# Kernel tuning notes

Measured on AMD Instinct MI355X. Metric: run time of the kernel, lower is better.

Reference implementation:

```python
import jax, jax.numpy as jnp
import numpy as np

METAPATH = [0, 1, 2]
NUM_REL = 5
N_NODES = 50000
N_EDGES = 800000
IN_DIM = 96
HID_DIM = 96
OUT_DIM = 96
LL_DIM = 64


def setup_inputs() -> dict:
    key = jax.random.key(0)
    ks = jax.random.split(key, 12)
    x = jax.random.normal(ks[0], (N_NODES, IN_DIM), dtype=jnp.float32)
    edge_index = jax.random.randint(ks[1], (2, N_EDGES), 0, N_NODES, dtype=jnp.int64)
    edge_type = jax.random.randint(ks[2], (N_EDGES,), 0, NUM_REL, dtype=jnp.int64)
    s1 = 1.0 / np.sqrt(IN_DIM)
    s2 = 1.0 / np.sqrt(HID_DIM)
    s3 = 1.0 / np.sqrt(OUT_DIM)
    w1 = jax.random.normal(ks[3], (NUM_REL, IN_DIM, HID_DIM), dtype=jnp.float32) * s1
    root1 = jax.random.normal(ks[4], (IN_DIM, HID_DIM), dtype=jnp.float32) * s1
    b1 = jnp.zeros((HID_DIM,), dtype=jnp.float32)
    w2 = jax.random.normal(ks[5], (NUM_REL, HID_DIM, OUT_DIM), dtype=jnp.float32) * s2
    root2 = jax.random.normal(ks[6], (HID_DIM, OUT_DIM), dtype=jnp.float32) * s2
    b2 = jnp.zeros((OUT_DIM,), dtype=jnp.float32)
    lin_w = jax.random.normal(ks[7], (OUT_DIM, LL_DIM), dtype=jnp.float32) * s3
    lin_b = jnp.zeros((LL_DIM,), dtype=jnp.float32)
    return {"x": x, "edge_index": edge_index, "edge_type": edge_type,
            "w1": w1, "root1": root1, "b1": b1,
            "w2": w2, "root2": root2, "b2": b2,
            "lin_w": lin_w, "lin_b": lin_b}


def _rgcn_layer(rel, h, edge_index, edge_type, W, root, bias):
    # flow='target_to_source': message from dst node, aggregated at src node.
    src, dst = edge_index[0], edge_index[1]
    mask = (edge_type == rel)
    msg = h[dst] @ W[rel]                      # [E, out] gather + per-relation GEMM
    msg = jnp.where(mask[:, None], msg, 0.0)
    agg = jax.ops.segment_sum(msg, src, num_segments=h.shape[0])   # scatter-add
    cnt = jax.ops.segment_sum(mask.astype(h.dtype), src, num_segments=h.shape[0])
    agg = agg / jnp.clip(cnt, 1.0)[:, None]    # mean normalization per target
    return agg + h @ root + bias


def reference(x, edge_index, edge_type, w1, root1, b1, w2, root2, b2, lin_w, lin_b):
    h = x
    for layer_index, rel in enumerate(METAPATH):
        if layer_index == 0:
            h = jax.nn.relu(_rgcn_layer(rel, h, edge_index, edge_type, w1, root1, b1))
        else:
            h = jax.nn.relu(_rgcn_layer(rel, h, edge_index, edge_type, w2, root2, b2))
    return h @ lin_w + lin_b
```

## Files before the change

### kernel.cpp

```cpp
#include <hip/hip_runtime.h>

#define NNODES 50000
#define NEDGES 800000
#define DIM 96
#define LLDIM 64
#define NRELS 3
#define SCAN_N (NRELS * NNODES)

#define BT_PLANE 18432
#define BT_LAYER (2 * BT_PLANE)
#define BTL_PLANE 6144
#define BT_LIN_OFF (3 * BT_LAYER)

typedef __attribute__((ext_vector_type(8))) short bf16x8;
typedef __attribute__((ext_vector_type(4))) float f32x4;

__device__ __forceinline__ unsigned short f2bf(float x) {
    union { float f; unsigned u; } v; v.f = x;
    unsigned r = v.u + 0x7fffu + ((v.u >> 16) & 1u);
    return (unsigned short)(r >> 16);
}
__device__ __forceinline__ float bf2f(unsigned short b) {
    union { unsigned u; float f; } v; v.u = ((unsigned)b) << 16;
    return v.f;
}


__global__ void hist_kernel(const int* __restrict__ ei, const int* __restrict__ et,
                            int* __restrict__ deg) {
    int e = blockIdx.x * 256 + threadIdx.x;
    if (e >= NEDGES) return;
    int r = et[e];
    if (r < NRELS) atomicAdd(&deg[r * NNODES + ei[e]], 1);
}

__global__ void scan1_kernel(const int* __restrict__ in, int* __restrict__ out,
                             int* __restrict__ partials, int n) {
    __shared__ int sdata[256];
    int tid = threadIdx.x;
    int base = blockIdx.x * 1024 + tid * 4;
    int v0 = (base + 0 < n) ? in[base + 0] : 0;
    int v1 = (base + 1 < n) ? in[base + 1] : 0;
    int v2 = (base + 2 < n) ? in[base + 2] : 0;
    int v3 = (base + 3 < n) ? in[base + 3] : 0;
    int tsum = v0 + v1 + v2 + v3;
    sdata[tid] = tsum;
    __syncthreads();
    for (int off = 1; off < 256; off <<= 1) {
        int x = sdata[tid];
        int y = (tid >= off) ? sdata[tid - off] : 0;
        __syncthreads();
        sdata[tid] = x + y;
        __syncthreads();
    }
    int excl = sdata[tid] - tsum;
    if (tid == 255) partials[blockIdx.x] = sdata[255];
    if (base + 0 < n) out[base + 0] = excl;
    excl += v0;
    if (base + 1 < n) out[base + 1] = excl;
    excl += v1;
    if (base + 2 < n) out[base + 2] = excl;
    excl += v2;
    if (base + 3 < n) out[base + 3] = excl;
}

__global__ void scan2_kernel(int* __restrict__ partials, int nb) {
    __shared__ int sdata[256];
    int tid = threadIdx.x;
    int v = (tid < nb) ? partials[tid] : 0;
    sdata[tid] = v;
    __syncthreads();
    for (int off = 1; off < 256; off <<= 1) {
        int x = sdata[tid];
        int y = (tid >= off) ? sdata[tid - off] : 0;
        __syncthreads();
        sdata[tid] = x + y;
        __syncthreads();
    }
    partials[tid] = sdata[tid] - v;
}

__global__ void scan3_kernel(int* __restrict__ out, int* __restrict__ cursor,
                             const int* __restrict__ partials, int n) {
    int idx = blockIdx.x * 256 + threadIdx.x;
    if (idx < n) {
        int v = out[idx] + partials[idx >> 10];
        out[idx] = v;
        cursor[idx] = v;
    }
}

__global__ void fill_kernel(const int* __restrict__ ei, const int* __restrict__ et,
                            int* __restrict__ cursor, int* __restrict__ col) {
    int e = blockIdx.x * 256 + threadIdx.x;
    if (e >= NEDGES) return;
    int r = et[e];
    if (r < NRELS) {
        int pos = atomicAdd(&cursor[r * NNODES + ei[e]], 1);
        col[pos] = ei[NEDGES + e];
    }
}


__global__ void prep_kernel(const float* __restrict__ w1, const float* __restrict__ root1,
                            const float* __restrict__ w2, const float* __restrict__ root2,
                            const float* __restrict__ lin_w,
                            unsigned short* __restrict__ bt, int* __restrict__ deg) {
    int idx = blockIdx.x * 256 + threadIdx.x;
    if (idx < SCAN_N) deg[idx] = 0;
    const int LYR = 96 * 192;
    if (idx < 3 * LYR) {
        int l = idx / LYR;
        int rem = idx % LYR;
        int c = rem / 192;
        int k = rem % 192;
        const float* Wm;
        const float* Rm;
        if (l == 0) { Wm = w1; Rm = root1; }
        else        { Wm = w2 + (size_t)l * 96 * 96; Rm = root2; }
        float v = (k < 96) ? Wm[(size_t)k * 96 + c] : Rm[(size_t)(k - 96) * 96 + c];
        unsigned short hi = f2bf(v);
        unsigned short lo = f2bf(v - bf2f(hi));
        int ph = k / 96, kk = k % 96;
        int ks = kk / 32, g = (kk & 31) >> 3, kr = k & 7;
        int cg = c >> 4, r = c & 15;
        size_t off = (((size_t)((ph * 3 + ks) * 6 + cg)) * 64 + g * 16 + r) * 8 + kr;
        unsigned short* base = bt + (size_t)l * BT_LAYER;
        base[off] = hi;
        base[BT_PLANE + off] = lo;
    } else if (idx < 3 * LYR + 64 * 96) {
        int rem = idx - 3 * LYR;
        int c = rem / 96;
        int k = rem % 96;
        float v = lin_w[(size_t)k * 64 + c];
        unsigned short hi = f2bf(v);
        unsigned short lo = f2bf(v - bf2f(hi));
        int ks = k / 32, g = (k & 31) >> 3, kr = k & 7;
        int cg = c >> 4, r = c & 15;
        size_t off = (((size_t)(ks * 4 + cg)) * 64 + g * 16 + r) * 8 + kr;
        unsigned short* base = bt + BT_LIN_OFF;
        base[off] = hi;
        base[BTL_PLANE + off] = lo;
    }
}


__device__ __forceinline__ void gather_to_lds(
    const float* __restrict__ h, const int* __restrict__ rs, const int* __restrict__ re,
    const int* __restrict__ col, int n0, int tid,
    unsigned short* Ah, unsigned short* Al) {
    const int nd = tid >> 2;
    const int node = n0 + nd;
    const int cq4 = (tid & 3) * 24;
    float a[24];
#pragma unroll
    for (int j = 0; j < 24; ++j) a[j] = 0.0f;
    int s = 0, e = 0;
    if (node < NNODES) { s = rs[node]; e = re[node]; }
    for (int i = s; i < e; ++i) {
        int d = col[i];
        const float* p = h + (size_t)d * DIM + cq4;
#pragma unroll
        for (int j6 = 0; j6 < 6; ++j6) {
            float4 v = *(const float4*)(p + j6 * 4);
            a[j6 * 4 + 0] += v.x; a[j6 * 4 + 1] += v.y;
            a[j6 * 4 + 2] += v.z; a[j6 * 4 + 3] += v.w;
        }
    }
    float scl = 1.0f / fmaxf((float)(e - s), 1.0f);
    int arow = nd * 104 + cq4;
#pragma unroll
    for (int jp = 0; jp < 12; ++jp) {
        float v0 = a[jp * 2] * scl, v1 = a[jp * 2 + 1] * scl;
        unsigned short h0 = f2bf(v0), h1 = f2bf(v1);
        unsigned short l0 = f2bf(v0 - bf2f(h0)), l1 = f2bf(v1 - bf2f(h1));
        *(unsigned int*)&Ah[arow + jp * 2] = (unsigned)h0 | ((unsigned)h1 << 16);
        *(unsigned int*)&Al[arow + jp * 2] = (unsigned)l0 | ((unsigned)l1 << 16);
    }
}

__device__ __forceinline__ void stage_h_to_lds(
    const float* __restrict__ src, int n0, int tid,
    unsigned short* Ah, unsigned short* Al) {
#pragma unroll
    for (int j = 0; j < 6; ++j) {
        int idx = tid + j * 256;
        int nd = idx / 24;
        int kq = idx % 24;
        int node = n0 + nd;
        if (node >= NNODES) node = NNODES - 1;
        float4 v = *(const float4*)(src + (size_t)node * DIM + kq * 4);
        unsigned short h0 = f2bf(v.x), h1 = f2bf(v.y), h2 = f2bf(v.z), h3 = f2bf(v.w);
        *(ushort4*)&Ah[nd * 104 + kq * 4] = make_ushort4(h0, h1, h2, h3);
        unsigned short l0 = f2bf(v.x - bf2f(h0));
        unsigned short l1 = f2bf(v.y - bf2f(h1));
        unsigned short l2 = f2bf(v.z - bf2f(h2));
        unsigned short l3 = f2bf(v.w - bf2f(h3));
        *(ushort4*)&Al[nd * 104 + kq * 4] = make_ushort4(l0, l1, l2, l3);
    }
}

#define KS_LOOP(PH)                                                                     \
    _Pragma("unroll")                                                                   \
    for (int ks = 0; ks < 3; ++ks) {                                                    \
        const int ko = ks * 32 + g * 8;                                                 \
        bf16x8 a0h = *(const bf16x8*)&Ah[(rb_base + r) * 104 + ko];                     \
        bf16x8 a1h = *(const bf16x8*)&Ah[(rb_base + 16 + r) * 104 + ko];                \
        bf16x8 a0l = *(const bf16x8*)&Al[(rb_base + r) * 104 + ko];                     \
        bf16x8 a1l = *(const bf16x8*)&Al[(rb_base + 16 + r) * 104 + ko];                \
        const unsigned short* bks = bt + ((size_t)(((PH) * 3 + ks) * 6) * 64 + lane) * 8;\
        _Pragma("unroll")                                                               \
        for (int ct = 0; ct < 3; ++ct) {                                                \
            const unsigned short* bp = bks + (size_t)(cg_base + ct) * 512;              \
            bf16x8 bhv = *(const bf16x8*)bp;                                            \
            bf16x8 blv = *(const bf16x8*)(bp + BT_PLANE);                               \
            acc[0][ct] = __builtin_amdgcn_mfma_f32_16x16x32_bf16(a0h, bhv, acc[0][ct], 0, 0, 0); \
            acc[1][ct] = __builtin_amdgcn_mfma_f32_16x16x32_bf16(a1h, bhv, acc[1][ct], 0, 0, 0); \
            acc[0][ct] = __builtin_amdgcn_mfma_f32_16x16x32_bf16(a0l, bhv, acc[0][ct], 0, 0, 0); \
            acc[1][ct] = __builtin_amdgcn_mfma_f32_16x16x32_bf16(a1l, bhv, acc[1][ct], 0, 0, 0); \
            acc[0][ct] = __builtin_amdgcn_mfma_f32_16x16x32_bf16(a0h, blv, acc[0][ct], 0, 0, 0); \
            acc[1][ct] = __builtin_amdgcn_mfma_f32_16x16x32_bf16(a1h, blv, acc[1][ct], 0, 0, 0); \
        }                                                                               \
    }

__global__ __launch_bounds__(256) void layer_fused_kernel(
    const float* __restrict__ h, const int* __restrict__ rs, const int* __restrict__ re,
    const int* __restrict__ col, const unsigned short* __restrict__ bt,
    const float* __restrict__ b, float* __restrict__ out) {
    __shared__ unsigned short Ah[64 * 104];
    __shared__ unsigned short Al[64 * 104];
    const int tid = threadIdx.x;
    const int lane = tid & 63;
    const int w = tid >> 6;
    const int r = lane & 15;
    const int g = lane >> 4;
    const int rb_base = (w >> 1) * 32;
    const int cg_base = (w & 1) * 3;
    const int n0 = blockIdx.x * 64;

    gather_to_lds(h, rs, re, col, n0, tid, Ah, Al);

    f32x4 acc[2][3];
#pragma unroll
    for (int i = 0; i < 2; ++i)
#pragma unroll
        for (int j = 0; j < 3; ++j) acc[i][j] = (f32x4){0.f, 0.f, 0.f, 0.f};

    __syncthreads();
    KS_LOOP(0)
    __syncthreads();
    stage_h_to_lds(h, n0, tid, Ah, Al);
    __syncthreads();
    KS_LOOP(1)

#pragma unroll
    for (int ct = 0; ct < 3; ++ct) {
        int colc = (cg_base + ct) * 16 + r;
        float bias = b[colc];
#pragma unroll
        for (int rbi = 0; rbi < 2; ++rbi) {
            int row0 = n0 + rb_base + rbi * 16 + g * 4;
#pragma unroll
            for (int j = 0; j < 4; ++j) {
                int node = row0 + j;
                if (node < NNODES)
                    out[(size_t)node * DIM + colc] = fmaxf(acc[rbi][ct][j] + bias, 0.0f);
            }
        }
    }
}


__global__ __launch_bounds__(256) void layer2_final_kernel(
    const float* __restrict__ h, const int* __restrict__ rs, const int* __restrict__ re,
    const int* __restrict__ col, const unsigned short* __restrict__ bt,
    const float* __restrict__ b, const unsigned short* __restrict__ btl,
    const float* __restrict__ LB, float* __restrict__ out) {
    __shared__ unsigned short Ah[64 * 104];
    __shared__ unsigned short Al[64 * 104];
    const int tid = threadIdx.x;
    const int lane = tid & 63;
    const int w = tid >> 6;
    const int r = lane & 15;
    const int g = lane >> 4;
    const int rb_base = (w >> 1) * 32;
    const int cg_base = (w & 1) * 3;
    const int n0 = blockIdx.x * 64;

    gather_to_lds(h, rs, re, col, n0, tid, Ah, Al);

    f32x4 acc[2][3];
#pragma unroll
    for (int i = 0; i < 2; ++i)
#pragma unroll
        for (int j = 0; j < 3; ++j) acc[i][j] = (f32x4){0.f, 0.f, 0.f, 0.f};

    __syncthreads();
    KS_LOOP(0)
    __syncthreads();
    stage_h_to_lds(h, n0, tid, Ah, Al);
    __syncthreads();
    KS_LOOP(1)

    __syncthreads();
#pragma unroll
    for (int ct = 0; ct < 3; ++ct) {
        int colc = (cg_base + ct) * 16 + r;
        float bias = b[colc];
#pragma unroll
        for (int rbi = 0; rbi < 2; ++rbi) {
            int row0 = rb_base + rbi * 16 + g * 4;
#pragma unroll
            for (int j = 0; j < 4; ++j) {
                float v = fmaxf(acc[rbi][ct][j] + bias, 0.0f);
                unsigned short hh = f2bf(v);
                unsigned short ll = f2bf(v - bf2f(hh));
                Ah[(row0 + j) * 104 + colc] = hh;
                Al[(row0 + j) * 104 + colc] = ll;
            }
        }
    }
    __syncthreads();

    const int cgf = (w & 1) * 2;
    f32x4 accf[2][2];
#pragma unroll
    for (int i = 0; i < 2; ++i)
#pragma unroll
        for (int j = 0; j < 2; ++j) accf[i][j] = (f32x4){0.f, 0.f, 0.f, 0.f};

#pragma unroll
    for (int ks = 0; ks < 3; ++ks) {
        const int ko = ks * 32 + g * 8;
        bf16x8 a0h = *(const bf16x8*)&Ah[(rb_base + r) * 104 + ko];
        bf16x8 a1h = *(const bf16x8*)&Ah[(rb_base + 16 + r) * 104 + ko];
        bf16x8 a0l = *(const bf16x8*)&Al[(rb_base + r) * 104 + ko];
        bf16x8 a1l = *(const bf16x8*)&Al[(rb_base + 16 + r) * 104 + ko];
        const unsigned short* bks = btl + ((size_t)(ks * 4) * 64 + lane) * 8;
#pragma unroll
        for (int ct = 0; ct < 2; ++ct) {
            const unsigned short* bp = bks + (size_t)(cgf + ct) * 512;
            bf16x8 bhv = *(const bf16x8*)bp;
            bf16x8 blv = *(const bf16x8*)(bp + BTL_PLANE);
            accf[0][ct] = __builtin_amdgcn_mfma_f32_16x16x32_bf16(a0h, bhv, accf[0][ct], 0, 0, 0);
            accf[1][ct] = __builtin_amdgcn_mfma_f32_16x16x32_bf16(a1h, bhv, accf[1][ct], 0, 0, 0);
            accf[0][ct] = __builtin_amdgcn_mfma_f32_16x16x32_bf16(a0l, bhv, accf[0][ct], 0, 0, 0);
            accf[1][ct] = __builtin_amdgcn_mfma_f32_16x16x32_bf16(a1l, bhv, accf[1][ct], 0, 0, 0);
            accf[0][ct] = __builtin_amdgcn_mfma_f32_16x16x32_bf16(a0h, blv, accf[0][ct], 0, 0, 0);
            accf[1][ct] = __builtin_amdgcn_mfma_f32_16x16x32_bf16(a1h, blv, accf[1][ct], 0, 0, 0);
        }
    }

#pragma unroll
    for (int ct = 0; ct < 2; ++ct) {
        int colc = (cgf + ct) * 16 + r;
        float bias = LB[colc];
#pragma unroll
        for (int rbi = 0; rbi < 2; ++rbi) {
            int row0 = n0 + rb_base + rbi * 16 + g * 4;
#pragma unroll
            for (int j = 0; j < 4; ++j) {
                int node = row0 + j;
                if (node < NNODES)
                    out[(size_t)node * LLDIM + colc] = accf[rbi][ct][j] + bias;
            }
        }
    }
}

extern "C" void kernel_launch(void* const* d_in, const int* in_sizes, int n_in,
                              void* d_out, int out_size, void* d_ws, size_t ws_size,
                              hipStream_t stream) {
    const float* x     = (const float*)d_in[0];
    const int*   ei    = (const int*)d_in[1];
    const int*   et    = (const int*)d_in[2];
    const float* w1    = (const float*)d_in[3];
    const float* root1 = (const float*)d_in[4];
    const float* b1    = (const float*)d_in[5];
    const float* w2    = (const float*)d_in[6];
    const float* root2 = (const float*)d_in[7];
    const float* b2    = (const float*)d_in[8];
    const float* lin_w = (const float*)d_in[9];
    const float* lin_b = (const float*)d_in[10];

    float* bufA = (float*)d_ws;
    float* bufB = bufA + (size_t)NNODES * DIM;
    int* deg       = (int*)(bufB + (size_t)NNODES * DIM);
    int* row_start = deg + SCAN_N;
    int* row_end   = row_start + SCAN_N;
    int* col       = row_end + SCAN_N;
    int* partials  = col + NEDGES;
    unsigned short* bt = (unsigned short*)(partials + 256);

    const int edge_blocks = (NEDGES + 255) / 256;
    const int scan_blocks = (SCAN_N + 1023) / 1024;
    const int node_tiles  = (NNODES + 63) / 64;
    const int prep_blocks = (SCAN_N + 255) / 256;

    prep_kernel<<<prep_blocks, 256, 0, stream>>>(w1, root1, w2, root2, lin_w, bt, deg);

    hist_kernel<<<edge_blocks, 256, 0, stream>>>(ei, et, deg);
    scan1_kernel<<<scan_blocks, 256, 0, stream>>>(deg, row_start, partials, SCAN_N);
    scan2_kernel<<<1, 256, 0, stream>>>(partials, scan_blocks);
    scan3_kernel<<<(SCAN_N + 255) / 256, 256, 0, stream>>>(row_start, row_end, partials, SCAN_N);
    fill_kernel<<<edge_blocks, 256, 0, stream>>>(ei, et, row_end, col);

    layer_fused_kernel<<<node_tiles, 256, 0, stream>>>(
        x, row_start + 0 * NNODES, row_end + 0 * NNODES, col,
        bt + 0 * (size_t)BT_LAYER, b1, bufA);

    layer_fused_kernel<<<node_tiles, 256, 0, stream>>>(
        bufA, row_start + 1 * NNODES, row_end + 1 * NNODES, col,
        bt + 1 * (size_t)BT_LAYER, b2, bufB);

    layer2_final_kernel<<<node_tiles, 256, 0, stream>>>(
        bufB, row_start + 2 * NNODES, row_end + 2 * NNODES, col,
        bt + 2 * (size_t)BT_LAYER, b2, bt + BT_LIN_OFF, lin_b, (float*)d_out);
}
```

Measured before the change: 221.3 us.

## Double threads per node tile and unroll neighbor gather by two

The three layer kernels now launch 512 threads per 64-node tile instead of 256. Each node's gather is split across 8 threads with 12 columns each, and the edge loop is unrolled by two with separate accumulators so more loads are in flight. The MFMA work per wave drops to one 16-row block. This aims to raise memory-level parallelism in the latency-bound neighbor gather, at the cost of more waves competing for the same LDS tile and redundant B-fragment loads per wave.

```diff
diff --git a/kernel.cpp b/kernel.cpp
--- a/kernel.cpp
+++ b/kernel.cpp
@@ -149,28 +149,46 @@
     const float* __restrict__ h, const int* __restrict__ rs, const int* __restrict__ re,
     const int* __restrict__ col, int n0, int tid,
     unsigned short* Ah, unsigned short* Al) {
-    const int nd = tid >> 2;
+    const int nd = tid >> 3;
     const int node = n0 + nd;
-    const int cq4 = (tid & 3) * 24;
-    float a[24];
-#pragma unroll
-    for (int j = 0; j < 24; ++j) a[j] = 0.0f;
+    const int cq = (tid & 7) * 12;
+    float a[12], b[12];
+#pragma unroll
+    for (int j = 0; j < 12; ++j) { a[j] = 0.0f; b[j] = 0.0f; }
     int s = 0, e = 0;
     if (node < NNODES) { s = rs[node]; e = re[node]; }
-    for (int i = s; i < e; ++i) {
+    int i = s;
+    for (; i + 2 <= e; i += 2) {
+        int d0 = col[i];
+        int d1 = col[i + 1];
+        const float* p0 = h + (size_t)d0 * DIM + cq;
+        const float* p1 = h + (size_t)d1 * DIM + cq;
+#pragma unroll
+        for (int j4 = 0; j4 < 3; ++j4) {
+            float4 v0 = *(const float4*)(p0 + j4 * 4);
+            float4 v1 = *(const float4*)(p1 + j4 * 4);
+            a[j4 * 4 + 0] += v0.x; a[j4 * 4 + 1] += v0.y;
+            a[j4 * 4 + 2] += v0.z; a[j4 * 4 + 3] += v0.w;
+            b[j4 * 4 + 0] += v1.x; b[j4 * 4 + 1] += v1.y;
+            b[j4 * 4 + 2] += v1.z; b[j4 * 4 + 3] += v1.w;
+        }
+    }
+    if (i < e) {
         int d = col[i];
-        const float* p = h + (size_t)d * DIM + cq4;
-#pragma unroll
-        for (int j6 = 0; j6 < 6; ++j6) {
-            float4 v = *(const float4*)(p + j6 * 4);
-            a[j6 * 4 + 0] += v.x; a[j6 * 4 + 1] += v.y;
-            a[j6 * 4 + 2] += v.z; a[j6 * 4 + 3] += v.w;
-        }
-    }
+        const float* p = h + (size_t)d * DIM + cq;
+#pragma unroll
+        for (int j4 = 0; j4 < 3; ++j4) {
+            float4 v = *(const float4*)(p + j4 * 4);
+            a[j4 * 4 + 0] += v.x; a[j4 * 4 + 1] += v.y;
+            a[j4 * 4 + 2] += v.z; a[j4 * 4 + 3] += v.w;
+        }
+    }
+#pragma unroll
+    for (int j = 0; j < 12; ++j) a[j] += b[j];
     float scl = 1.0f / fmaxf((float)(e - s), 1.0f);
-    int arow = nd * 104 + cq4;
-#pragma unroll
-    for (int jp = 0; jp < 12; ++jp) {
+    int arow = nd * 104 + cq;
+#pragma unroll
+    for (int jp = 0; jp < 6; ++jp) {
         float v0 = a[jp * 2] * scl, v1 = a[jp * 2 + 1] * scl;
         unsigned short h0 = f2bf(v0), h1 = f2bf(v1);
         unsigned short l0 = f2bf(v0 - bf2f(h0)), l1 = f2bf(v1 - bf2f(h1));
@@ -183,8 +201,8 @@
     const float* __restrict__ src, int n0, int tid,
     unsigned short* Ah, unsigned short* Al) {
 #pragma unroll
-    for (int j = 0; j < 6; ++j) {
-        int idx = tid + j * 256;
+    for (int j = 0; j < 3; ++j) {
+        int idx = tid + j * 512;
         int nd = idx / 24;
         int kq = idx % 24;
         int node = n0 + nd;
@@ -205,25 +223,20 @@
     for (int ks = 0; ks < 3; ++ks) {                                                    \
         const int ko = ks * 32 + g * 8;                                                 \
         bf16x8 a0h = *(const bf16x8*)&Ah[(rb_base + r) * 104 + ko];                     \
-        bf16x8 a1h = *(const bf16x8*)&Ah[(rb_base + 16 + r) * 104 + ko];                \
         bf16x8 a0l = *(const bf16x8*)&Al[(rb_base + r) * 104 + ko];                     \
-        bf16x8 a1l = *(const bf16x8*)&Al[(rb_base + 16 + r) * 104 + ko];                \
         const unsigned short* bks = bt + ((size_t)(((PH) * 3 + ks) * 6) * 64 + lane) * 8;\
         _Pragma("unroll")                                                               \
         for (int ct = 0; ct < 3; ++ct) {                                                \
             const unsigned short* bp = bks + (size_t)(cg_base + ct) * 512;              \
             bf16x8 bhv = *(const bf16x8*)bp;                                            \
             bf16x8 blv = *(const bf16x8*)(bp + BT_PLANE);                               \
-            acc[0][ct] = __builtin_amdgcn_mfma_f32_16x16x32_bf16(a0h, bhv, acc[0][ct], 0, 0, 0); \
-            acc[1][ct] = __builtin_amdgcn_mfma_f32_16x16x32_bf16(a1h, bhv, acc[1][ct], 0, 0, 0); \
-            acc[0][ct] = __builtin_amdgcn_mfma_f32_16x16x32_bf16(a0l, bhv, acc[0][ct], 0, 0, 0); \
-            acc[1][ct] = __builtin_amdgcn_mfma_f32_16x16x32_bf16(a1l, bhv, acc[1][ct], 0, 0, 0); \
-            acc[0][ct] = __builtin_amdgcn_mfma_f32_16x16x32_bf16(a0h, blv, acc[0][ct], 0, 0, 0); \
-            acc[1][ct] = __builtin_amdgcn_mfma_f32_16x16x32_bf16(a1h, blv, acc[1][ct], 0, 0, 0); \
+            acc[ct] = __builtin_amdgcn_mfma_f32_16x16x32_bf16(a0h, bhv, acc[ct], 0, 0, 0); \
+            acc[ct] = __builtin_amdgcn_mfma_f32_16x16x32_bf16(a0l, bhv, acc[ct], 0, 0, 0); \
+            acc[ct] = __builtin_amdgcn_mfma_f32_16x16x32_bf16(a0h, blv, acc[ct], 0, 0, 0); \
         }                                                                               \
     }
 
-__global__ __launch_bounds__(256) void layer_fused_kernel(
+__global__ __launch_bounds__(512, 4) void layer_fused_kernel(
     const float* __restrict__ h, const int* __restrict__ rs, const int* __restrict__ re,
     const int* __restrict__ col, const unsigned short* __restrict__ bt,
     const float* __restrict__ b, float* __restrict__ out) {
@@ -234,17 +247,15 @@
     const int w = tid >> 6;
     const int r = lane & 15;
     const int g = lane >> 4;
-    const int rb_base = (w >> 1) * 32;
+    const int rb_base = (w >> 1) * 16;
     const int cg_base = (w & 1) * 3;
     const int n0 = blockIdx.x * 64;
 
     gather_to_lds(h, rs, re, col, n0, tid, Ah, Al);
 
-    f32x4 acc[2][3];
-#pragma unroll
-    for (int i = 0; i < 2; ++i)
-#pragma unroll
-        for (int j = 0; j < 3; ++j) acc[i][j] = (f32x4){0.f, 0.f, 0.f, 0.f};
+    f32x4 acc[3];
+#pragma unroll
+    for (int j = 0; j < 3; ++j) acc[j] = (f32x4){0.f, 0.f, 0.f, 0.f};
 
     __syncthreads();
     KS_LOOP(0)
@@ -257,21 +268,18 @@
     for (int ct = 0; ct < 3; ++ct) {
         int colc = (cg_base + ct) * 16 + r;
         float bias = b[colc];
-#pragma unroll
-        for (int rbi = 0; rbi < 2; ++rbi) {
-            int row0 = n0 + rb_base + rbi * 16 + g * 4;
-#pragma unroll
-            for (int j = 0; j < 4; ++j) {
-                int node = row0 + j;
-                if (node < NNODES)
-                    out[(size_t)node * DIM + colc] = fmaxf(acc[rbi][ct][j] + bias, 0.0f);
-            }
-        }
-    }
-}
-
-
-__global__ __launch_bounds__(256) void layer2_final_kernel(
+        int row0 = n0 + rb_base + g * 4;
+#pragma unroll
+        for (int j = 0; j < 4; ++j) {
+            int node = row0 + j;
+            if (node < NNODES)
+                out[(size_t)node * DIM + colc] = fmaxf(acc[ct][j] + bias, 0.0f);
+        }
+    }
+}
+
+
+__global__ __launch_bounds__(512, 4) void layer2_final_kernel(
     const float* __restrict__ h, const int* __restrict__ rs, const int* __restrict__ re,
     const int* __restrict__ col, const unsigned short* __restrict__ bt,
     const float* __restrict__ b, const unsigned short* __restrict__ btl,
@@ -283,17 +291,15 @@
     const int w = tid >> 6;
     const int r = lane & 15;
     const int g = lane >> 4;
-    const int rb_base = (w >> 1) * 32;
+    const int rb_base = (w >> 1) * 16;
     const int cg_base = (w & 1) * 3;
     const int n0 = blockIdx.x * 64;
 
     gather_to_lds(h, rs, re, col, n0, tid, Ah, Al);
 
-    f32x4 acc[2][3];
-#pragma unroll
-    for (int i = 0; i < 2; ++i)
-#pragma unroll
-        for (int j = 0; j < 3; ++j) acc[i][j] = (f32x4){0.f, 0.f, 0.f, 0.f};
+    f32x4 acc[3];
+#pragma unroll
+    for (int j = 0; j < 3; ++j) acc[j] = (f32x4){0.f, 0.f, 0.f, 0.f};
 
     __syncthreads();
     KS_LOOP(0)
@@ -307,47 +313,37 @@
     for (int ct = 0; ct < 3; ++ct) {
         int colc = (cg_base + ct) * 16 + r;
         float bias = b[colc];
-#pragma unroll
-        for (int rbi = 0; rbi < 2; ++rbi) {
-            int row0 = rb_base + rbi * 16 + g * 4;
-#pragma unroll
-            for (int j = 0; j < 4; ++j) {
-                float v = fmaxf(acc[rbi][ct][j] + bias, 0.0f);
-                unsigned short hh = f2bf(v);
-                unsigned short ll = f2bf(v - bf2f(hh));
-                Ah[(row0 + j) * 104 + colc] = hh;
-                Al[(row0 + j) * 104 + colc] = ll;
-            }
+        int row0 = rb_base + g * 4;
+#pragma unroll
+        for (int j = 0; j < 4; ++j) {
+            float v = fmaxf(acc[ct][j] + bias, 0.0f);
+            unsigned short hh = f2bf(v);
+            unsigned short ll = f2bf(v - bf2f(hh));
+            Ah[(row0 + j) * 104 + colc] = hh;
+            Al[(row0 + j) * 104 + colc] = ll;
         }
     }
     __syncthreads();
 
     const int cgf = (w & 1) * 2;
-    f32x4 accf[2][2];
-#pragma unroll
-    for (int i = 0; i < 2; ++i)
-#pragma unroll
-        for (int j = 0; j < 2; ++j) accf[i][j] = (f32x4){0.f, 0.f, 0.f, 0.f};
+    f32x4 accf[2];
+#pragma unroll
+    for (int j = 0; j < 2; ++j) accf[j] = (f32x4){0.f, 0.f, 0.f, 0.f};
 
 #pragma unroll
     for (int ks = 0; ks < 3; ++ks) {
         const int ko = ks * 32 + g * 8;
         bf16x8 a0h = *(const bf16x8*)&Ah[(rb_base + r) * 104 + ko];
-        bf16x8 a1h = *(const bf16x8*)&Ah[(rb_base + 16 + r) * 104 + ko];
         bf16x8 a0l = *(const bf16x8*)&Al[(rb_base + r) * 104 + ko];
-        bf16x8 a1l = *(const bf16x8*)&Al[(rb_base + 16 + r) * 104 + ko];
         const unsigned short* bks = btl + ((size_t)(ks * 4) * 64 + lane) * 8;
 #pragma unroll
         for (int ct = 0; ct < 2; ++ct) {
             const unsigned short* bp = bks + (size_t)(cgf + ct) * 512;
             bf16x8 bhv = *(const bf16x8*)bp;
             bf16x8 blv = *(const bf16x8*)(bp + BTL_PLANE);
-            accf[0][ct] = __builtin_amdgcn_mfma_f32_16x16x32_bf16(a0h, bhv, accf[0][ct], 0, 0, 0);
-            accf[1][ct] = __builtin_amdgcn_mfma_f32_16x16x32_bf16(a1h, bhv, accf[1][ct], 0, 0, 0);
-            accf[0][ct] = __builtin_amdgcn_mfma_f32_16x16x32_bf16(a0l, bhv, accf[0][ct], 0, 0, 0);
-            accf[1][ct] = __builtin_amdgcn_mfma_f32_16x16x32_bf16(a1l, bhv, accf[1][ct], 0, 0, 0);
-            accf[0][ct] = __builtin_amdgcn_mfma_f32_16x16x32_bf16(a0h, blv, accf[0][ct], 0, 0, 0);
-            accf[1][ct] = __builtin_amdgcn_mfma_f32_16x16x32_bf16(a1h, blv, accf[1][ct], 0, 0, 0);
+            accf[ct] = __builtin_amdgcn_mfma_f32_16x16x32_bf16(a0h, bhv, accf[ct], 0, 0, 0);
+            accf[ct] = __builtin_amdgcn_mfma_f32_16x16x32_bf16(a0l, bhv, accf[ct], 0, 0, 0);
+            accf[ct] = __builtin_amdgcn_mfma_f32_16x16x32_bf16(a0h, blv, accf[ct], 0, 0, 0);
         }
     }
 
@@ -355,15 +351,12 @@
     for (int ct = 0; ct < 2; ++ct) {
         int colc = (cgf + ct) * 16 + r;
         float bias = LB[colc];
-#pragma unroll
-        for (int rbi = 0; rbi < 2; ++rbi) {
-            int row0 = n0 + rb_base + rbi * 16 + g * 4;
-#pragma unroll
-            for (int j = 0; j < 4; ++j) {
-                int node = row0 + j;
-                if (node < NNODES)
-                    out[(size_t)node * LLDIM + colc] = accf[rbi][ct][j] + bias;
-            }
+        int row0 = n0 + rb_base + g * 4;
+#pragma unroll
+        for (int j = 0; j < 4; ++j) {
+            int node = row0 + j;
+            if (node < NNODES)
+                out[(size_t)node * LLDIM + colc] = accf[ct][j] + bias;
         }
     }
 }
@@ -405,15 +398,15 @@
     scan3_kernel<<<(SCAN_N + 255) / 256, 256, 0, stream>>>(row_start, row_end, partials, SCAN_N);
     fill_kernel<<<edge_blocks, 256, 0, stream>>>(ei, et, row_end, col);
 
-    layer_fused_kernel<<<node_tiles, 256, 0, stream>>>(
+    layer_fused_kernel<<<node_tiles, 512, 0, stream>>>(
         x, row_start + 0 * NNODES, row_end + 0 * NNODES, col,
         bt + 0 * (size_t)BT_LAYER, b1, bufA);
 
-    layer_fused_kernel<<<node_tiles, 256, 0, stream>>>(
+    layer_fused_kernel<<<node_tiles, 512, 0, stream>>>(
         bufA, row_start + 1 * NNODES, row_end + 1 * NNODES, col,
         bt + 1 * (size_t)BT_LAYER, b2, bufB);
 
-    layer2_final_kernel<<<node_tiles, 256, 0, stream>>>(
+    layer2_final_kernel<<<node_tiles, 512, 0, stream>>>(
         bufB, row_start + 2 * NNODES, row_end + 2 * NNODES, col,
         bt + 2 * (size_t)BT_LAYER, b2, bt + BT_LIN_OFF, lin_b, (float*)d_out);
 }
```

New measurement: 232.2 us. 1.05x slower.

## Load root operand directly from global into MFMA registers and drop scan2 kernel

Applied to the files above, without the earlier changes.

The self (root) GEMM phase no longer stages h into LDS with two extra barriers. Each lane loads its A fragments straight from global memory and splits them into bf16 hi/lo in registers. Separately, the single-block scan2 launch is removed: each scan3 block now reduces the preceding block partials itself, which saves a kernel launch at the cost of redundant reductions. The direct loads are less coalesced (8 floats per lane per row) and repeat across the two column-group waves.

```diff
diff --git a/kernel.cpp b/kernel.cpp
--- a/kernel.cpp
+++ b/kernel.cpp
@@ -23,6 +23,16 @@
 __device__ __forceinline__ float bf2f(unsigned short b) {
     union { unsigned u; float f; } v; v.u = ((unsigned)b) << 16;
     return v.f;
+}
+__device__ __forceinline__ void f8_to_bf(const float* f, bf16x8& hv, bf16x8& lv) {
+    union { bf16x8 v; unsigned short u[8]; } H, L;
+#pragma unroll
+    for (int j = 0; j < 8; ++j) {
+        unsigned short hh = f2bf(f[j]);
+        H.u[j] = hh;
+        L.u[j] = f2bf(f[j] - bf2f(hh));
+    }
+    hv = H.v; lv = L.v;
 }
 
 
@@ -64,27 +74,21 @@
     if (base + 3 < n) out[base + 3] = excl;
 }
 
-__global__ void scan2_kernel(int* __restrict__ partials, int nb) {
+__global__ void scan3_kernel(int* __restrict__ out, int* __restrict__ cursor,
+                             const int* __restrict__ partials, int n) {
     __shared__ int sdata[256];
     int tid = threadIdx.x;
-    int v = (tid < nb) ? partials[tid] : 0;
-    sdata[tid] = v;
-    __syncthreads();
-    for (int off = 1; off < 256; off <<= 1) {
-        int x = sdata[tid];
-        int y = (tid >= off) ? sdata[tid - off] : 0;
+    int c = blockIdx.x >> 2;
+    sdata[tid] = (tid < c) ? partials[tid] : 0;
+    __syncthreads();
+    for (int off = 128; off > 0; off >>= 1) {
+        if (tid < off) sdata[tid] += sdata[tid + off];
         __syncthreads();
-        sdata[tid] = x + y;
-        __syncthreads();
-    }
-    partials[tid] = sdata[tid] - v;
-}
-
-__global__ void scan3_kernel(int* __restrict__ out, int* __restrict__ cursor,
-                             const int* __restrict__ partials, int n) {
-    int idx = blockIdx.x * 256 + threadIdx.x;
+    }
+    int base = sdata[0];
+    int idx = blockIdx.x * 256 + tid;
     if (idx < n) {
-        int v = out[idx] + partials[idx >> 10];
+        int v = out[idx] + base;
         out[idx] = v;
         cursor[idx] = v;
     }
@@ -179,28 +183,7 @@
     }
 }
 
-__device__ __forceinline__ void stage_h_to_lds(
-    const float* __restrict__ src, int n0, int tid,
-    unsigned short* Ah, unsigned short* Al) {
-#pragma unroll
-    for (int j = 0; j < 6; ++j) {
-        int idx = tid + j * 256;
-        int nd = idx / 24;
-        int kq = idx % 24;
-        int node = n0 + nd;
-        if (node >= NNODES) node = NNODES - 1;
-        float4 v = *(const float4*)(src + (size_t)node * DIM + kq * 4);
-        unsigned short h0 = f2bf(v.x), h1 = f2bf(v.y), h2 = f2bf(v.z), h3 = f2bf(v.w);
-        *(ushort4*)&Ah[nd * 104 + kq * 4] = make_ushort4(h0, h1, h2, h3);
-        unsigned short l0 = f2bf(v.x - bf2f(h0));
-        unsigned short l1 = f2bf(v.y - bf2f(h1));
-        unsigned short l2 = f2bf(v.z - bf2f(h2));
-        unsigned short l3 = f2bf(v.w - bf2f(h3));
-        *(ushort4*)&Al[nd * 104 + kq * 4] = make_ushort4(l0, l1, l2, l3);
-    }
-}
-
-#define KS_LOOP(PH)                                                                     \
+#define KS_LOOP0                                                                        \
     _Pragma("unroll")                                                                   \
     for (int ks = 0; ks < 3; ++ks) {                                                    \
         const int ko = ks * 32 + g * 8;                                                 \
@@ -208,7 +191,34 @@
         bf16x8 a1h = *(const bf16x8*)&Ah[(rb_base + 16 + r) * 104 + ko];                \
         bf16x8 a0l = *(const bf16x8*)&Al[(rb_base + r) * 104 + ko];                     \
         bf16x8 a1l = *(const bf16x8*)&Al[(rb_base + 16 + r) * 104 + ko];                \
-        const unsigned short* bks = bt + ((size_t)(((PH) * 3 + ks) * 6) * 64 + lane) * 8;\
+        const unsigned short* bks = bt + ((size_t)(ks * 6) * 64 + lane) * 8;            \
+        _Pragma("unroll")                                                               \
+        for (int ct = 0; ct < 3; ++ct) {                                                \
+            const unsigned short* bp = bks + (size_t)(cg_base + ct) * 512;              \
+            bf16x8 bhv = *(const bf16x8*)bp;                                            \
+            bf16x8 blv = *(const bf16x8*)(bp + BT_PLANE);                               \
+            acc[0][ct] = __builtin_amdgcn_mfma_f32_16x16x32_bf16(a0h, bhv, acc[0][ct], 0, 0, 0); \
+            acc[1][ct] = __builtin_amdgcn_mfma_f32_16x16x32_bf16(a1h, bhv, acc[1][ct], 0, 0, 0); \
+            acc[0][ct] = __builtin_amdgcn_mfma_f32_16x16x32_bf16(a0l, bhv, acc[0][ct], 0, 0, 0); \
+            acc[1][ct] = __builtin_amdgcn_mfma_f32_16x16x32_bf16(a1l, bhv, acc[1][ct], 0, 0, 0); \
+            acc[0][ct] = __builtin_amdgcn_mfma_f32_16x16x32_bf16(a0h, blv, acc[0][ct], 0, 0, 0); \
+            acc[1][ct] = __builtin_amdgcn_mfma_f32_16x16x32_bf16(a1h, blv, acc[1][ct], 0, 0, 0); \
+        }                                                                               \
+    }
+
+#define KS_LOOP1                                                                        \
+    _Pragma("unroll")                                                                   \
+    for (int ks = 0; ks < 3; ++ks) {                                                    \
+        const int ko = ks * 32 + g * 8;                                                 \
+        float f0[8], f1[8];                                                             \
+        *(float4*)&f0[0] = *(const float4*)(h + (size_t)row0g * DIM + ko);              \
+        *(float4*)&f0[4] = *(const float4*)(h + (size_t)row0g * DIM + ko + 4);          \
+        *(float4*)&f1[0] = *(const float4*)(h + (size_t)row1g * DIM + ko);              \
+        *(float4*)&f1[4] = *(const float4*)(h + (size_t)row1g * DIM + ko + 4);          \
+        bf16x8 a0h, a0l, a1h, a1l;                                                      \
+        f8_to_bf(f0, a0h, a0l);                                                         \
+        f8_to_bf(f1, a1h, a1l);                                                         \
+        const unsigned short* bks = bt + ((size_t)((3 + ks) * 6) * 64 + lane) * 8;      \
         _Pragma("unroll")                                                               \
         for (int ct = 0; ct < 3; ++ct) {                                                \
             const unsigned short* bp = bks + (size_t)(cg_base + ct) * 512;              \
@@ -246,12 +256,12 @@
 #pragma unroll
         for (int j = 0; j < 3; ++j) acc[i][j] = (f32x4){0.f, 0.f, 0.f, 0.f};
 
-    __syncthreads();
-    KS_LOOP(0)
-    __syncthreads();
-    stage_h_to_lds(h, n0, tid, Ah, Al);
-    __syncthreads();
-    KS_LOOP(1)
+    int row0g = n0 + rb_base + r;      if (row0g >= NNODES) row0g = NNODES - 1;
+    int row1g = n0 + rb_base + 16 + r; if (row1g >= NNODES) row1g = NNODES - 1;
+
+    __syncthreads();
+    KS_LOOP0
+    KS_LOOP1
 
 #pragma unroll
     for (int ct = 0; ct < 3; ++ct) {
@@ -295,12 +305,12 @@
 #pragma unroll
         for (int j = 0; j < 3; ++j) acc[i][j] = (f32x4){0.f, 0.f, 0.f, 0.f};
 
-    __syncthreads();
-    KS_LOOP(0)
-    __syncthreads();
-    stage_h_to_lds(h, n0, tid, Ah, Al);
-    __syncthreads();
-    KS_LOOP(1)
+    int row0g = n0 + rb_base + r;      if (row0g >= NNODES) row0g = NNODES - 1;
+    int row1g = n0 + rb_base + 16 + r; if (row1g >= NNODES) row1g = NNODES - 1;
+
+    __syncthreads();
+    KS_LOOP0
+    KS_LOOP1
 
     __syncthreads();
 #pragma unroll
@@ -401,7 +411,6 @@
 
     hist_kernel<<<edge_blocks, 256, 0, stream>>>(ei, et, deg);
     scan1_kernel<<<scan_blocks, 256, 0, stream>>>(deg, row_start, partials, SCAN_N);
-    scan2_kernel<<<1, 256, 0, stream>>>(partials, scan_blocks);
     scan3_kernel<<<(SCAN_N + 255) / 256, 256, 0, stream>>>(row_start, row_end, partials, SCAN_N);
     fill_kernel<<<edge_blocks, 256, 0, stream>>>(ei, et, row_end, col);
 
```

New measurement: 229.8 us. +3.8%, slower.

## Double layer block threads, split gather across edges, run root and message GEMMs in parallel

Applied to the files above, without the earlier changes.

The fused layer kernels now launch 512 threads per 64-node tile. Each node's edge list is split between two thread groups and the partial sums are combined with a shuffle. Half the waves compute the aggregated-message GEMM while the other half compute the root GEMM at the same time, and the two results are reduced through LDS, which removes the serialized second phase. The scan2 kernel is folded into scan3, where each block reduces the preceding block partials itself, and the final linear layer is spread across 8 waves. This costs twice the LDS per block and an extra reduction sync, which may lower occupancy.

```diff
diff --git a/kernel.cpp b/kernel.cpp
--- a/kernel.cpp
+++ b/kernel.cpp
@@ -64,27 +64,21 @@
     if (base + 3 < n) out[base + 3] = excl;
 }
 
-__global__ void scan2_kernel(int* __restrict__ partials, int nb) {
+__global__ void scan3_kernel(int* __restrict__ out, int* __restrict__ cursor,
+                             const int* __restrict__ partials, int n) {
     __shared__ int sdata[256];
     int tid = threadIdx.x;
-    int v = (tid < nb) ? partials[tid] : 0;
-    sdata[tid] = v;
-    __syncthreads();
-    for (int off = 1; off < 256; off <<= 1) {
-        int x = sdata[tid];
-        int y = (tid >= off) ? sdata[tid - off] : 0;
+    int c = blockIdx.x >> 2;
+    sdata[tid] = (tid < c) ? partials[tid] : 0;
+    __syncthreads();
+    for (int off = 128; off > 0; off >>= 1) {
+        if (tid < off) sdata[tid] += sdata[tid + off];
         __syncthreads();
-        sdata[tid] = x + y;
-        __syncthreads();
-    }
-    partials[tid] = sdata[tid] - v;
-}
-
-__global__ void scan3_kernel(int* __restrict__ out, int* __restrict__ cursor,
-                             const int* __restrict__ partials, int n) {
-    int idx = blockIdx.x * 256 + threadIdx.x;
+    }
+    int base = sdata[0];
+    int idx = blockIdx.x * 256 + tid;
     if (idx < n) {
-        int v = out[idx] + partials[idx >> 10];
+        int v = out[idx] + base;
         out[idx] = v;
         cursor[idx] = v;
     }
@@ -145,21 +139,44 @@
 }
 
 
-__device__ __forceinline__ void gather_to_lds(
+__device__ __forceinline__ void stage_h_512(
+    const float* __restrict__ h, int n0, int tid,
+    unsigned short* Hh, unsigned short* Hl) {
+#pragma unroll
+    for (int j = 0; j < 3; ++j) {
+        int idx = tid + j * 512;
+        int nd = idx / 24;
+        int kq = idx % 24;
+        int node = n0 + nd;
+        if (node >= NNODES) node = NNODES - 1;
+        float4 v = *(const float4*)(h + (size_t)node * DIM + kq * 4);
+        unsigned short h0 = f2bf(v.x), h1 = f2bf(v.y), h2 = f2bf(v.z), h3 = f2bf(v.w);
+        *(ushort4*)&Hh[nd * 104 + kq * 4] = make_ushort4(h0, h1, h2, h3);
+        unsigned short l0 = f2bf(v.x - bf2f(h0));
+        unsigned short l1 = f2bf(v.y - bf2f(h1));
+        unsigned short l2 = f2bf(v.z - bf2f(h2));
+        unsigned short l3 = f2bf(v.w - bf2f(h3));
+        *(ushort4*)&Hl[nd * 104 + kq * 4] = make_ushort4(l0, l1, l2, l3);
+    }
+}
+
+__device__ __forceinline__ void gather_512(
     const float* __restrict__ h, const int* __restrict__ rs, const int* __restrict__ re,
     const int* __restrict__ col, int n0, int tid,
-    unsigned short* Ah, unsigned short* Al) {
-    const int nd = tid >> 2;
+    unsigned short* Gh, unsigned short* Gl) {
+    const int nd = tid >> 3;
     const int node = n0 + nd;
-    const int cq4 = (tid & 3) * 24;
+    const int j = tid & 7;
+    const int cq = (j & 3) * 24;
+    const int es = j >> 2;
     float a[24];
 #pragma unroll
-    for (int j = 0; j < 24; ++j) a[j] = 0.0f;
+    for (int m = 0; m < 24; ++m) a[m] = 0.0f;
     int s = 0, e = 0;
     if (node < NNODES) { s = rs[node]; e = re[node]; }
-    for (int i = s; i < e; ++i) {
+    for (int i = s + es; i < e; i += 2) {
         int d = col[i];
-        const float* p = h + (size_t)d * DIM + cq4;
+        const float* p = h + (size_t)d * DIM + cq;
 #pragma unroll
         for (int j6 = 0; j6 < 6; ++j6) {
             float4 v = *(const float4*)(p + j6 * 4);
@@ -167,47 +184,29 @@
             a[j6 * 4 + 2] += v.z; a[j6 * 4 + 3] += v.w;
         }
     }
+#pragma unroll
+    for (int m = 0; m < 24; ++m) a[m] += __shfl_xor(a[m], 4);
     float scl = 1.0f / fmaxf((float)(e - s), 1.0f);
-    int arow = nd * 104 + cq4;
-#pragma unroll
-    for (int jp = 0; jp < 12; ++jp) {
-        float v0 = a[jp * 2] * scl, v1 = a[jp * 2 + 1] * scl;
+    const int cb = es * 12;
+    int arow = nd * 104 + cq + cb;
+#pragma unroll
+    for (int jp = 0; jp < 6; ++jp) {
+        float v0 = a[cb + jp * 2] * scl, v1 = a[cb + jp * 2 + 1] * scl;
         unsigned short h0 = f2bf(v0), h1 = f2bf(v1);
         unsigned short l0 = f2bf(v0 - bf2f(h0)), l1 = f2bf(v1 - bf2f(h1));
-        *(unsigned int*)&Ah[arow + jp * 2] = (unsigned)h0 | ((unsigned)h1 << 16);
-        *(unsigned int*)&Al[arow + jp * 2] = (unsigned)l0 | ((unsigned)l1 << 16);
-    }
-}
-
-__device__ __forceinline__ void stage_h_to_lds(
-    const float* __restrict__ src, int n0, int tid,
-    unsigned short* Ah, unsigned short* Al) {
-#pragma unroll
-    for (int j = 0; j < 6; ++j) {
-        int idx = tid + j * 256;
-        int nd = idx / 24;
-        int kq = idx % 24;
-        int node = n0 + nd;
-        if (node >= NNODES) node = NNODES - 1;
-        float4 v = *(const float4*)(src + (size_t)node * DIM + kq * 4);
-        unsigned short h0 = f2bf(v.x), h1 = f2bf(v.y), h2 = f2bf(v.z), h3 = f2bf(v.w);
-        *(ushort4*)&Ah[nd * 104 + kq * 4] = make_ushort4(h0, h1, h2, h3);
-        unsigned short l0 = f2bf(v.x - bf2f(h0));
-        unsigned short l1 = f2bf(v.y - bf2f(h1));
-        unsigned short l2 = f2bf(v.z - bf2f(h2));
-        unsigned short l3 = f2bf(v.w - bf2f(h3));
-        *(ushort4*)&Al[nd * 104 + kq * 4] = make_ushort4(l0, l1, l2, l3);
-    }
-}
-
-#define KS_LOOP(PH)                                                                     \
+        *(unsigned int*)&Gh[arow + jp * 2] = (unsigned)h0 | ((unsigned)h1 << 16);
+        *(unsigned int*)&Gl[arow + jp * 2] = (unsigned)l0 | ((unsigned)l1 << 16);
+    }
+}
+
+#define KS_PHASE(AH, AL, PH)                                                            \
     _Pragma("unroll")                                                                   \
     for (int ks = 0; ks < 3; ++ks) {                                                    \
         const int ko = ks * 32 + g * 8;                                                 \
-        bf16x8 a0h = *(const bf16x8*)&Ah[(rb_base + r) * 104 + ko];                     \
-        bf16x8 a1h = *(const bf16x8*)&Ah[(rb_base + 16 + r) * 104 + ko];                \
-        bf16x8 a0l = *(const bf16x8*)&Al[(rb_base + r) * 104 + ko];                     \
-        bf16x8 a1l = *(const bf16x8*)&Al[(rb_base + 16 + r) * 104 + ko];                \
+        bf16x8 a0h = *(const bf16x8*)&AH[(rb_base + r) * 104 + ko];                     \
+        bf16x8 a1h = *(const bf16x8*)&AH[(rb_base + 16 + r) * 104 + ko];                \
+        bf16x8 a0l = *(const bf16x8*)&AL[(rb_base + r) * 104 + ko];                     \
+        bf16x8 a1l = *(const bf16x8*)&AL[(rb_base + 16 + r) * 104 + ko];                \
         const unsigned short* bks = bt + ((size_t)(((PH) * 3 + ks) * 6) * 64 + lane) * 8;\
         _Pragma("unroll")                                                               \
         for (int ct = 0; ct < 3; ++ct) {                                                \
@@ -223,22 +222,28 @@
         }                                                                               \
     }
 
-__global__ __launch_bounds__(256) void layer_fused_kernel(
+__global__ __launch_bounds__(512) void layer_fused_kernel(
     const float* __restrict__ h, const int* __restrict__ rs, const int* __restrict__ re,
     const int* __restrict__ col, const unsigned short* __restrict__ bt,
     const float* __restrict__ b, float* __restrict__ out) {
-    __shared__ unsigned short Ah[64 * 104];
-    __shared__ unsigned short Al[64 * 104];
+    __shared__ unsigned short SM[4 * 64 * 104];
+    unsigned short* Gh = SM;
+    unsigned short* Gl = SM + 6656;
+    unsigned short* Hh = SM + 2 * 6656;
+    unsigned short* Hl = SM + 3 * 6656;
     const int tid = threadIdx.x;
     const int lane = tid & 63;
     const int w = tid >> 6;
+    const int wq = w & 3;
+    const int pp = w >> 2;
     const int r = lane & 15;
     const int g = lane >> 4;
-    const int rb_base = (w >> 1) * 32;
-    const int cg_base = (w & 1) * 3;
+    const int rb_base = (wq >> 1) * 32;
+    const int cg_base = (wq & 1) * 3;
     const int n0 = blockIdx.x * 64;
 
-    gather_to_lds(h, rs, re, col, n0, tid, Ah, Al);
+    stage_h_512(h, n0, tid, Hh, Hl);
+    gather_512(h, rs, re, col, n0, tid, Gh, Gl);
 
     f32x4 acc[2][3];
 #pragma unroll
@@ -247,47 +252,76 @@
         for (int j = 0; j < 3; ++j) acc[i][j] = (f32x4){0.f, 0.f, 0.f, 0.f};
 
     __syncthreads();
-    KS_LOOP(0)
-    __syncthreads();
-    stage_h_to_lds(h, n0, tid, Ah, Al);
-    __syncthreads();
-    KS_LOOP(1)
-
-#pragma unroll
-    for (int ct = 0; ct < 3; ++ct) {
-        int colc = (cg_base + ct) * 16 + r;
-        float bias = b[colc];
-#pragma unroll
-        for (int rbi = 0; rbi < 2; ++rbi) {
-            int row0 = n0 + rb_base + rbi * 16 + g * 4;
-#pragma unroll
-            for (int j = 0; j < 4; ++j) {
-                int node = row0 + j;
-                if (node < NNODES)
-                    out[(size_t)node * DIM + colc] = fmaxf(acc[rbi][ct][j] + bias, 0.0f);
+    if (pp == 0) { KS_PHASE(Gh, Gl, 0) }
+    else         { KS_PHASE(Hh, Hl, 1) }
+    __syncthreads();
+
+    float* X = (float*)SM;
+    if (pp) {
+        int t = tid - 256;
+#pragma unroll
+        for (int i = 0; i < 2; ++i)
+#pragma unroll
+            for (int ct = 0; ct < 3; ++ct) {
+                int o = t * 26 + (i * 3 + ct) * 4;
+                *(float2*)&X[o]     = make_float2(acc[i][ct][0], acc[i][ct][1]);
+                *(float2*)&X[o + 2] = make_float2(acc[i][ct][2], acc[i][ct][3]);
+            }
+    }
+    __syncthreads();
+    if (pp == 0) {
+#pragma unroll
+        for (int i = 0; i < 2; ++i)
+#pragma unroll
+            for (int ct = 0; ct < 3; ++ct) {
+                int o = tid * 26 + (i * 3 + ct) * 4;
+                float2 u0 = *(float2*)&X[o];
+                float2 u1 = *(float2*)&X[o + 2];
+                acc[i][ct][0] += u0.x; acc[i][ct][1] += u0.y;
+                acc[i][ct][2] += u1.x; acc[i][ct][3] += u1.y;
+            }
+#pragma unroll
+        for (int ct = 0; ct < 3; ++ct) {
+            int colc = (cg_base + ct) * 16 + r;
+            float bias = b[colc];
+#pragma unroll
+            for (int rbi = 0; rbi < 2; ++rbi) {
+                int row0 = n0 + rb_base + rbi * 16 + g * 4;
+#pragma unroll
+                for (int j = 0; j < 4; ++j) {
+                    int node = row0 + j;
+                    if (node < NNODES)
+                        out[(size_t)node * DIM + colc] = fmaxf(acc[rbi][ct][j] + bias, 0.0f);
+                }
             }
         }
     }
 }
 
 
-__global__ __launch_bounds__(256) void layer2_final_kernel(
+__global__ __launch_bounds__(512) void layer2_final_kernel(
     const float* __restrict__ h, const int* __restrict__ rs, const int* __restrict__ re,
     const int* __restrict__ col, const unsigned short* __restrict__ bt,
     const float* __restrict__ b, const unsigned short* __restrict__ btl,
     const float* __restrict__ LB, float* __restrict__ out) {
-    __shared__ unsigned short Ah[64 * 104];
-    __shared__ unsigned short Al[64 * 104];
+    __shared__ unsigned short SM[4 * 64 * 104];
+    unsigned short* Gh = SM;
+    unsigned short* Gl = SM + 6656;
+    unsigned short* Hh = SM + 2 * 6656;
+    unsigned short* Hl = SM + 3 * 6656;
     const int tid = threadIdx.x;
     const int lane = tid & 63;
     const int w = tid >> 6;
+    const int wq = w & 3;
+    const int pp = w >> 2;
     const int r = lane & 15;
     const int g = lane >> 4;
-    const int rb_base = (w >> 1) * 32;
-    const int cg_base = (w & 1) * 3;
+    const int rb_base = (wq >> 1) * 32;
+    const int cg_base = (wq & 1) * 3;
     const int n0 = blockIdx.x * 64;
 
-    gather_to_lds(h, rs, re, col, n0, tid, Ah, Al);
+    stage_h_512(h, n0, tid, Hh, Hl);
+    gather_512(h, rs, re, col, n0, tid, Gh, Gl);
 
     f32x4 acc[2][3];
 #pragma unroll
@@ -296,73 +330,84 @@
         for (int j = 0; j < 3; ++j) acc[i][j] = (f32x4){0.f, 0.f, 0.f, 0.f};
 
     __syncthreads();
-    KS_LOOP(0)
-    __syncthreads();
-    stage_h_to_lds(h, n0, tid, Ah, Al);
-    __syncthreads();
-    KS_LOOP(1)
-
-    __syncthreads();
-#pragma unroll
-    for (int ct = 0; ct < 3; ++ct) {
-        int colc = (cg_base + ct) * 16 + r;
-        float bias = b[colc];
-#pragma unroll
-        for (int rbi = 0; rbi < 2; ++rbi) {
-            int row0 = rb_base + rbi * 16 + g * 4;
-#pragma unroll
-            for (int j = 0; j < 4; ++j) {
-                float v = fmaxf(acc[rbi][ct][j] + bias, 0.0f);
-                unsigned short hh = f2bf(v);
-                unsigned short ll = f2bf(v - bf2f(hh));
-                Ah[(row0 + j) * 104 + colc] = hh;
-                Al[(row0 + j) * 104 + colc] = ll;
+    if (pp == 0) { KS_PHASE(Gh, Gl, 0) }
+    else         { KS_PHASE(Hh, Hl, 1) }
+    __syncthreads();
+
+    float* X = (float*)SM;
+    if (pp) {
+        int t = tid - 256;
+#pragma unroll
+        for (int i = 0; i < 2; ++i)
+#pragma unroll
+            for (int ct = 0; ct < 3; ++ct) {
+                int o = t * 26 + (i * 3 + ct) * 4;
+                *(float2*)&X[o]     = make_float2(acc[i][ct][0], acc[i][ct][1]);
+                *(float2*)&X[o + 2] = make_float2(acc[i][ct][2], acc[i][ct][3]);
+            }
+    }
+    __syncthreads();
+    if (pp == 0) {
+#pragma unroll
+        for (int ct = 0; ct < 3; ++ct) {
+            int colc = (cg_base + ct) * 16 + r;
+            float bias = b[colc];
+#pragma unroll
+            for (int rbi = 0; rbi < 2; ++rbi) {
+                int o = tid * 26 + (rbi * 3 + ct) * 4;
+                float2 u0 = *(float2*)&X[o];
+                float2 u1 = *(float2*)&X[o + 2];
+                float vv[4] = {acc[rbi][ct][0] + u0.x, acc[rbi][ct][1] + u0.y,
+                               acc[rbi][ct][2] + u1.x, acc[rbi][ct][3] + u1.y};
+                int row0 = rb_base + rbi * 16 + g * 4;
+#pragma unroll
+                for (int j = 0; j < 4; ++j) {
+                    float v = fmaxf(vv[j] + bias, 0.0f);
+                    unsigned short hh = f2bf(v);
+                    unsigned short ll = f2bf(v - bf2f(hh));
+                    Hh[(row0 + j) * 104 + colc] = hh;
+                    Hl[(row0 + j) * 104 + colc] = ll;
+                }
             }
         }
     }
     __syncthreads();
 
-    const int cgf = (w & 1) * 2;
-    f32x4 accf[2][2];
-#pragma unroll
-    for (int i = 0; i < 2; ++i)
-#pragma unroll
-        for (int j = 0; j < 2; ++j) accf[i][j] = (f32x4){0.f, 0.f, 0.f, 0.f};
+    const int rbf = (w >> 2) * 32;
+    const int cgf = w & 3;
+    f32x4 accf[2];
+#pragma unroll
+    for (int j = 0; j < 2; ++j) accf[j] = (f32x4){0.f, 0.f, 0.f, 0.f};
 
 #pragma unroll
     for (int ks = 0; ks < 3; ++ks) {
         const int ko = ks * 32 + g * 8;
-        bf16x8 a0h = *(const bf16x8*)&Ah[(rb_base + r) * 104 + ko];
-        bf16x8 a1h = *(const bf16x8*)&Ah[(rb_base + 16 + r) * 104 + ko];
-        bf16x8 a0l = *(const bf16x8*)&Al[(rb_base + r) * 104 + ko];
-        bf16x8 a1l = *(const bf16x8*)&Al[(rb_base + 16 + r) * 104 + ko];
-        const unsigned short* bks = btl + ((size_t)(ks * 4) * 64 + lane) * 8;
-#pragma unroll
-        for (int ct = 0; ct < 2; ++ct) {
-            const unsigned short* bp = bks + (size_t)(cgf + ct) * 512;
-            bf16x8 bhv = *(const bf16x8*)bp;
-            bf16x8 blv = *(const bf16x8*)(bp + BTL_PLANE);
-            accf[0][ct] = __builtin_amdgcn_mfma_f32_16x16x32_bf16(a0h, bhv, accf[0][ct], 0, 0, 0);
-            accf[1][ct] = __builtin_amdgcn_mfma_f32_16x16x32_bf16(a1h, bhv, accf[1][ct], 0, 0, 0);
-            accf[0][ct] = __builtin_amdgcn_mfma_f32_16x16x32_bf16(a0l, bhv, accf[0][ct], 0, 0, 0);
-            accf[1][ct] = __builtin_amdgcn_mfma_f32_16x16x32_bf16(a1l, bhv, accf[1][ct], 0, 0, 0);
-            accf[0][ct] = __builtin_amdgcn_mfma_f32_16x16x32_bf16(a0h, blv, accf[0][ct], 0, 0, 0);
-            accf[1][ct] = __builtin_amdgcn_mfma_f32_16x16x32_bf16(a1h, blv, accf[1][ct], 0, 0, 0);
-        }
-    }
-
-#pragma unroll
-    for (int ct = 0; ct < 2; ++ct) {
-        int colc = (cgf + ct) * 16 + r;
+        bf16x8 a0h = *(const bf16x8*)&Hh[(rbf + r) * 104 + ko];
+        bf16x8 a1h = *(const bf16x8*)&Hh[(rbf + 16 + r) * 104 + ko];
+        bf16x8 a0l = *(const bf16x8*)&Hl[(rbf + r) * 104 + ko];
+        bf16x8 a1l = *(const bf16x8*)&Hl[(rbf + 16 + r) * 104 + ko];
+        const unsigned short* bp = btl + ((size_t)(ks * 4 + cgf) * 64 + lane) * 8;
+        bf16x8 bhv = *(const bf16x8*)bp;
+        bf16x8 blv = *(const bf16x8*)(bp + BTL_PLANE);
+        accf[0] = __builtin_amdgcn_mfma_f32_16x16x32_bf16(a0h, bhv, accf[0], 0, 0, 0);
+        accf[1] = __builtin_amdgcn_mfma_f32_16x16x32_bf16(a1h, bhv, accf[1], 0, 0, 0);
+        accf[0] = __builtin_amdgcn_mfma_f32_16x16x32_bf16(a0l, bhv, accf[0], 0, 0, 0);
+        accf[1] = __builtin_amdgcn_mfma_f32_16x16x32_bf16(a1l, bhv, accf[1], 0, 0, 0);
+        accf[0] = __builtin_amdgcn_mfma_f32_16x16x32_bf16(a0h, blv, accf[0], 0, 0, 0);
+        accf[1] = __builtin_amdgcn_mfma_f32_16x16x32_bf16(a1h, blv, accf[1], 0, 0, 0);
+    }
+
+    {
+        int colc = cgf * 16 + r;
         float bias = LB[colc];
 #pragma unroll
         for (int rbi = 0; rbi < 2; ++rbi) {
-            int row0 = n0 + rb_base + rbi * 16 + g * 4;
+            int row0 = n0 + rbf + rbi * 16 + g * 4;
 #pragma unroll
             for (int j = 0; j < 4; ++j) {
                 int node = row0 + j;
                 if (node < NNODES)
-                    out[(size_t)node * LLDIM + colc] = accf[rbi][ct][j] + bias;
+                    out[(size_t)node * LLDIM + colc] = accf[rbi][j] + bias;
             }
         }
     }
@@ -393,27 +438,25 @@
     unsigned short* bt = (unsigned short*)(partials + 256);
 
     const int edge_blocks = (NEDGES + 255) / 256;
-    const int scan_blocks = (SCAN_N + 1023) / 1024;
     const int node_tiles  = (NNODES + 63) / 64;
     const int prep_blocks = (SCAN_N + 255) / 256;
 
     prep_kernel<<<prep_blocks, 256, 0, stream>>>(w1, root1, w2, root2, lin_w, bt, deg);
 
     hist_kernel<<<edge_blocks, 256, 0, stream>>>(ei, et, deg);
-    scan1_kernel<<<scan_blocks, 256, 0, stream>>>(deg, row_start, partials, SCAN_N);
-    scan2_kernel<<<1, 256, 0, stream>>>(partials, scan_blocks);
+    scan1_kernel<<<(SCAN_N + 1023) / 1024, 256, 0, stream>>>(deg, row_start, partials, SCAN_N);
     scan3_kernel<<<(SCAN_N + 255) / 256, 256, 0, stream>>>(row_start, row_end, partials, SCAN_N);
     fill_kernel<<<edge_blocks, 256, 0, stream>>>(ei, et, row_end, col);
 
-    layer_fused_kernel<<<node_tiles, 256, 0, stream>>>(
+    layer_fused_kernel<<<node_tiles, 512, 0, stream>>>(
         x, row_start + 0 * NNODES, row_end + 0 * NNODES, col,
         bt + 0 * (size_t)BT_LAYER, b1, bufA);
 
-    layer_fused_kernel<<<node_tiles, 256, 0, stream>>>(
+    layer_fused_kernel<<<node_tiles, 512, 0, stream>>>(
         bufA, row_start + 1 * NNODES, row_end + 1 * NNODES, col,
         bt + 1 * (size_t)BT_LAYER, b2, bufB);
 
-    layer2_final_kernel<<<node_tiles, 256, 0, stream>>>(
+    layer2_final_kernel<<<node_tiles, 512, 0, stream>>>(
         bufB, row_start + 2 * NNODES, row_end + 2 * NNODES, col,
         bt + 2 * (size_t)BT_LAYER, b2, bt + BT_LIN_OFF, lin_b, (float*)d_out);
 }
```

New measurement: 239.9 us. +8.4%, slower.
